# Kernel optimization log

Measured on AMD Instinct MI355X. Metric: run time of the kernel, lower is better.

Reference implementation:

```python
import jax, jax.numpy as jnp
import numpy as np

EPS = 1e-5
K_NEIGH = 8


def _conv1(x, w, b):
    # x: [B,C,N], w: [O,C], b: [O] -> [B,O,N]  (1x1 Conv1d)
    return jnp.einsum('bcn,oc->bon', x, w) + b[None, :, None]


def _bn(x, g, b):
    # BatchNorm1d in training mode: stats over (B, N)
    m = jnp.mean(x, axis=(0, 2), keepdims=True)
    v = jnp.var(x, axis=(0, 2), keepdims=True)
    return g[None, :, None] * (x - m) * jax.lax.rsqrt(v + EPS) + b[None, :, None]


def _get_local_diffs(x, k):
    # x: [B,N,C] -> [B, 2C, N]
    xyz = x[:, :, :3]
    sq = jnp.sum(xyz * xyz, axis=-1)  # [B,N]
    d2 = sq[:, :, None] + sq[:, None, :] - 2.0 * jnp.einsum('bnc,bmc->bnm', xyz, xyz)
    dists = jnp.sqrt(jnp.maximum(d2, 0.0))  # [B,N,N]
    _, idx = jax.lax.top_k(-dists, k + 1)   # smallest distances
    idx = idx[:, :, 1:]                     # drop self -> [B,N,k]
    neigh = jax.vmap(lambda xi, ii: xi[ii])(x, idx)  # [B,N,k,C]
    diff_mean = jnp.mean(neigh, axis=2) - x          # [B,N,C]
    out = jnp.concatenate([diff_mean, x], axis=2)    # [B,N,2C]
    return jnp.transpose(out, (0, 2, 1))             # [B,2C,N]


def _forward(x, w1, b1, g1, be1, w2, b2, g2, be2, w3, b3, g3, be3,
             qw, qb, kw, kb, vw, vb, fw, fb, aw1, ab1, aw2, ab2, fcw, fcb):
    h = _get_local_diffs(x, K_NEIGH)                 # [B,18,N]
    h = jax.nn.relu(_bn(_conv1(h, w1, b1), g1, be1))  # [B,64,N]
    h = jax.nn.relu(_bn(_conv1(h, w2, b2), g2, be2))  # [B,128,N]
    h = jax.nn.relu(_bn(_conv1(h, w3, b3), g3, be3))  # [B,256,N]
    # global attention
    Q = _conv1(h, qw, qb)  # [B,H,N]
    Kt = _conv1(h, kw, kb)
    V = _conv1(h, vw, vb)
    attn = jax.nn.softmax(jnp.einsum('bhn,bhm->bnm', Q, Kt), axis=-1)  # [B,N,N]
    o = jnp.einsum('bhm,bnm->bhn', V, attn)
    h = _conv1(o, fw, fb) + h
    # attention pooling
    a = jax.nn.relu(_conv1(h, aw1, ab1))
    s = _conv1(a, aw2, ab2)                 # [B,1,N]
    w = jax.nn.softmax(s, axis=-1)
    pooled = jnp.sum(h * w, axis=-1)        # [B,256]
    return jax.nn.relu(pooled @ fcw.T + fcb)  # [B,256]


def setup_inputs() -> dict:
    key = jax.random.key(0)
    ks = jax.random.split(key, 32)
    B, N, C = 4, 4096, 9
    HID = 128

    def p(i, shape, scale=0.05):
        return (jax.random.normal(ks[i], shape, dtype=jnp.float32) * scale)

    inp = {'x': jax.random.normal(ks[0], (B, N, C), dtype=jnp.float32)}
    dims = [(2 * C, 64), (64, 128), (128, 256)]
    for li, (ci, co) in enumerate(dims, start=1):
        inp[f'w{li}'] = p(li, (co, ci))
        inp[f'b{li}'] = p(li + 3, (co,))
        inp[f'g{li}'] = jnp.ones((co,), jnp.float32)
        inp[f'be{li}'] = jnp.zeros((co,), jnp.float32)
    Cf = 256
    inp['qw'] = p(7, (HID, Cf)); inp['qb'] = p(8, (HID,))
    inp['kw'] = p(9, (HID, Cf)); inp['kb'] = p(10, (HID,))
    inp['vw'] = p(11, (HID, Cf)); inp['vb'] = p(12, (HID,))
    inp['fw'] = p(13, (Cf, HID)); inp['fb'] = p(14, (Cf,))
    inp['aw1'] = p(15, (64, Cf)); inp['ab1'] = p(16, (64,))
    inp['aw2'] = p(17, (1, 64)); inp['ab2'] = p(18, (1,))
    inp['fcw'] = p(19, (256, Cf)); inp['fcb'] = p(20, (256,))
    return inp


def reference(x, w1, b1, g1, be1, w2, b2, g2, be2, w3, b3, g3, be3,
              qw, qb, kw, kb, vw, vb, fw, fb, aw1, ab1, aw2, ab2, fcw, fcb):
    return _forward(x, w1, b1, g1, be1, w2, b2, g2, be2, w3, b3, g3, be3,
                    qw, qb, kw, kb, vw, vb, fw, fb, aw1, ab1, aw2, ab2, fcw, fcb)
```

## Files before the change

kernel.cpp:

```cpp
#include <hip/hip_runtime.h>
#include <math.h>

constexpr int B    = 4;
constexpr int NPTS = 4096;
constexpr int NTOT = B * NPTS;
constexpr int CIN  = 9;
constexpr int C0   = 18;
constexpr int KNB  = 8;
constexpr int HID  = 128;
constexpr int QR   = 64;
constexpr int KC   = 64;
constexpr int NSPL = 4;
constexpr float EPSF = 1e-5f;

using f32x4  = __attribute__((ext_vector_type(4))) float;
using bf16x8 = __attribute__((ext_vector_type(8))) short;

__device__ inline unsigned short f2bf(float f) {
    unsigned int x = __float_as_uint(f);
    unsigned int r = (x + 0x7fffu + ((x >> 16) & 1u)) >> 16;
    return (unsigned short)r;
}
__device__ inline float bf2f(unsigned short u) {
    return __uint_as_float(((unsigned int)u) << 16);
}
__device__ inline unsigned int pack2(float a, float b) {
    return (unsigned int)f2bf(a) | ((unsigned int)f2bf(b) << 16);
}

#define GLD_LDS16(g, l) __builtin_amdgcn_global_load_lds( \
    (const __attribute__((address_space(1))) void*)(g),   \
    (__attribute__((address_space(3))) void*)(l), 16, 0, 0)

__global__ __launch_bounds__(256) void prep_kernel(const float* __restrict__ x,
                                                   float4* __restrict__ xyzw,
                                                   const float* __restrict__ w2,
                                                   const float* __restrict__ w3,
                                                   const float* __restrict__ qw,
                                                   const float* __restrict__ kw,
                                                   const float* __restrict__ vw,
                                                   const float* __restrict__ fw,
                                                   const float* __restrict__ aw1,
                                                   unsigned short* __restrict__ dst) {
    const int i = blockIdx.x * 256 + threadIdx.x;
    if (i < NTOT) {
        const float* xp = x + (size_t)i * CIN;
        const float a = xp[0], b = xp[1], c = xp[2];
        xyzw[i] = make_float4(a, b, c, a * a + b * b + c * c);
    }
    const float* src;
    int off;
    if      (i <   8192) { src = w2;  off = 0; }
    else if (i <  40960) { src = w3;  off = 8192; }
    else if (i <  73728) { src = qw;  off = 40960; }
    else if (i < 106496) { src = kw;  off = 73728; }
    else if (i < 139264) { src = vw;  off = 106496; }
    else if (i < 172032) { src = fw;  off = 139264; }
    else                 { src = aw1; off = 172032; }
    dst[i] = f2bf(src[i - off]);
}

__global__ __launch_bounds__(256) void knn3_kernel(const float* __restrict__ x,
                                                   const float4* __restrict__ xyzw,
                                                   float* __restrict__ h0) {
    __shared__ __align__(16) char lds[16384];
    const int tid = threadIdx.x;
    const int w = tid >> 6, l = tid & 63;
    const int b  = blockIdx.x >> 9;
    const int p0 = (blockIdx.x & 511) << 3;
    const int c  = l & 31;
    const int p  = w * 2 + (l >> 5);
    const int n  = p0 + p;
    const float4* xb4 = xyzw + (size_t)b * NPTS;

    const float4 q4 = xb4[n];
    const float qx = q4.x, qy = q4.y, qz = q4.z, sqn = q4.w;

    float bd[KNB];
    int   bi[KNB];
#pragma unroll
    for (int i = 0; i < KNB; ++i) { bd[i] = 3.0e38f; bi[i] = 0; }

    auto stage = [&](int buf, int t) {
#pragma unroll
        for (int i = 0; i < 2; ++i) {
            const int idx = i * 256 + w * 64 + l;
            const int m   = idx ^ ((idx >> 4) & 7);
            GLD_LDS16(xb4 + (size_t)t * 512 + m, lds + buf * 8192 + i * 4096 + w * 1024);
        }
    };

    stage(0, 0);
    for (int t = 0; t < 8; ++t) {
        const int cur = t & 1;
        __syncthreads();
        if (t < 7) stage(cur ^ 1, t + 1);

        float thr = bd[KNB - 1];
        thr = fminf(thr, __shfl_xor(thr, 1));
        thr = fminf(thr, __shfl_xor(thr, 2));
        thr = fminf(thr, __shfl_xor(thr, 4));
        thr = fminf(thr, __shfl_xor(thr, 8));
        thr = fminf(thr, __shfl_xor(thr, 16));

        float gate = fminf(thr, bd[KNB - 1]);
        const char* buf = lds + cur * 8192 + c * 256;
        const int mbase = t * 512 + c * 16;
        const int cswz  = (c & 7) << 4;
#pragma unroll 4
        for (int j = 0; j < 16; ++j) {
            const float4 f4 = *(const float4*)(buf + ((j << 4) ^ cswz));
            const float tt = fmaf(qx, f4.x, fmaf(qy, f4.y, qz * f4.z));
            const float d2 = fmaf(-2.0f, tt, sqn + f4.w);
            const int m = mbase + j;
            const bool want = (d2 < gate) && (m != n);
            if (__any(want)) {
                if (want) {
                    bd[KNB - 1] = d2; bi[KNB - 1] = m;
#pragma unroll
                    for (int s = KNB - 1; s > 0; --s) {
                        if (bd[s] < bd[s - 1]) {
                            float td = bd[s]; bd[s] = bd[s - 1]; bd[s - 1] = td;
                            int   ti = bi[s]; bi[s] = bi[s - 1]; bi[s - 1] = ti;
                        }
                    }
                }
                gate = fminf(thr, bd[KNB - 1]);
            }
        }
    }

    int res[KNB];
    const int lh = l & 31;
#pragma unroll
    for (int r = 0; r < KNB; ++r) {
        float hd = bd[0]; int hb = bi[0]; int hl = lh;
#pragma unroll
        for (int mask = 16; mask > 0; mask >>= 1) {
            const float od = __shfl_xor(hd, mask);
            const int   ob = __shfl_xor(hb, mask);
            const int   ol = __shfl_xor(hl, mask);
            if (od < hd || (od == hd && ol < hl)) { hd = od; hb = ob; hl = ol; }
        }
        res[r] = hb;
        if (lh == hl) {
#pragma unroll
            for (int s = 0; s < KNB - 1; ++s) { bd[s] = bd[s + 1]; bi[s] = bi[s + 1]; }
            bd[KNB - 1] = 3.0e38f;
        }
    }

    const int c8 = c & 7;
    int nb = res[0];
#pragma unroll
    for (int k = 1; k < KNB; ++k) nb = (c8 == k) ? res[k] : nb;
    const float* xb = x + (size_t)b * NPTS * CIN;
    float nv[CIN];
    const float* nbp = xb + (size_t)nb * CIN;
#pragma unroll
    for (int ch = 0; ch < CIN; ++ch) nv[ch] = nbp[ch];
#pragma unroll
    for (int d = 1; d < 8; d <<= 1) {
#pragma unroll
        for (int ch = 0; ch < CIN; ++ch) nv[ch] += __shfl_xor(nv[ch], d);
    }
    const int ch = min(c, 8);
    float nvc = nv[0];
#pragma unroll
    for (int k = 1; k < CIN; ++k) nvc = (ch == k) ? nv[k] : nvc;
    if (c < 9) {
        const float xv = xb[(size_t)n * CIN + ch];
        h0[((size_t)b * C0 + ch) * NPTS + n]       = nvc * 0.125f - xv;
        h0[((size_t)b * C0 + CIN + ch) * NPTS + n] = xv;
    }
}

__global__ __launch_bounds__(256) void conv1_kernel(const float* __restrict__ X,
                                                    const float* __restrict__ W,
                                                    const float* __restrict__ bias,
                                                    float* __restrict__ Y,
                                                    float* __restrict__ parts) {
    __shared__ float Ws[16 * C0];
    const int b  = blockIdx.z;
    const int o_base = blockIdx.y * 16;
    const int l  = threadIdx.x & 63;
    const int n  = blockIdx.x * 64 + l;
    const int og = threadIdx.x >> 6;
    for (int i = threadIdx.x; i < 16 * C0; i += 256)
        Ws[i] = W[(size_t)o_base * C0 + i];
    __syncthreads();
    float acc[4] = {0.f, 0.f, 0.f, 0.f};
    const float* Xp = X + (size_t)b * C0 * NPTS + n;
    for (int c = 0; c < C0; ++c) {
        const float xv = Xp[(size_t)c * NPTS];
#pragma unroll
        for (int i = 0; i < 4; ++i)
            acc[i] = fmaf(Ws[(og * 4 + i) * C0 + c], xv, acc[i]);
    }
    f32x4 v;
#pragma unroll
    for (int i = 0; i < 4; ++i) v[i] = acc[i] + bias[o_base + og * 4 + i];
    *(f32x4*)(Y + ((size_t)b * NPTS + n) * 64 + o_base + og * 4) = v;
    float s1[4], s2[4];
#pragma unroll
    for (int i = 0; i < 4; ++i) { s1[i] = v[i]; s2[i] = v[i] * v[i]; }
#pragma unroll
    for (int d = 1; d < 64; d <<= 1) {
#pragma unroll
        for (int i = 0; i < 4; ++i) {
            s1[i] += __shfl_xor(s1[i], d);
            s2[i] += __shfl_xor(s2[i], d);
        }
    }
    if (l == 0) {
        const int rg = blockIdx.z * 64 + blockIdx.x;
#pragma unroll
        for (int i = 0; i < 4; ++i) {
            const int ch = o_base + og * 4 + i;
            parts[ch * 256 + rg]            = s1[i];
            parts[64 * 256 + ch * 256 + rg] = s2[i];
        }
    }
}

__global__ __launch_bounds__(64) void finstats_kernel(const float* __restrict__ parts,
                                                      float* __restrict__ mstats, int O) {
    const int ch = blockIdx.x, l = threadIdx.x;
    const f32x4 a1 = *(const f32x4*)(parts + (size_t)ch * 256 + l * 4);
    const f32x4 a2 = *(const f32x4*)(parts + (size_t)O * 256 + (size_t)ch * 256 + l * 4);
    float s1 = (a1[0] + a1[1]) + (a1[2] + a1[3]);
    float s2 = (a2[0] + a2[1]) + (a2[2] + a2[3]);
#pragma unroll
    for (int d = 1; d < 64; d <<= 1) {
        s1 += __shfl_xor(s1, d);
        s2 += __shfl_xor(s2, d);
    }
    if (l == 0) {
        const float mean = s1 * (1.0f / NTOT);
        const float var  = s2 * (1.0f / NTOT) - mean * mean;
        mstats[ch]     = mean;
        mstats[O + ch] = rsqrtf(var + EPSF);
    }
}

__global__ __launch_bounds__(256) void bnapply_kernel(const float* __restrict__ Y,
                                                      const float* __restrict__ mstats,
                                                      const float* __restrict__ g,
                                                      const float* __restrict__ be,
                                                      unsigned short* __restrict__ Yb,
                                                      int O) {
    const size_t i4 = (size_t)blockIdx.x * 256 + threadIdx.x;
    const int cbase = (int)((i4 * 4) & (O - 1));
    const f32x4 v = *(const f32x4*)(Y + i4 * 4);
    ushort4 pk;
    unsigned short* pp = (unsigned short*)&pk;
#pragma unroll
    for (int r = 0; r < 4; ++r) {
        const int c = cbase + r;
        const float y = fmaxf(g[c] * mstats[O + c] * (v[r] - mstats[c]) + be[c], 0.f);
        pp[r] = f2bf(y);
    }
    *(ushort4*)(Yb + i4 * 4) = pk;
}

template <int C, int EPI>
__global__ __launch_bounds__(256) void gemm_kernel(const unsigned short* __restrict__ A,
                                                   const unsigned short* __restrict__ Wb,
                                                   const float* __restrict__ bias,
                                                   const unsigned short* __restrict__ resid,
                                                   void* __restrict__ Yv, int O,
                                                   float* __restrict__ parts) {
    constexpr int RB = 2 * C;
    constexpr int SLOTS = C / 8;
    __shared__ __align__(16) char ldsW[64 * RB];
    const int tid = threadIdx.x;
    const int w = tid >> 6, l = tid & 63;
    const int lg = l >> 4, lq = l & 15;
    const int n0 = blockIdx.x * 64;
    const int o0 = blockIdx.y * 64;

#pragma unroll
    for (int i = 0; i < C / 32; ++i) {
        const int idx = i * 256 + tid;
        const int m  = idx / SLOTS;
        const int sl = (idx % SLOTS) ^ (m & 7);
        GLD_LDS16(Wb + (size_t)(o0 + m) * C + sl * 8, ldsW + (i * 256 + w * 64) * 16);
    }

    const int nr = n0 + w * 16 + lq;
    const unsigned short* Ap = A + (size_t)nr * C + lg * 8;
    f32x4 acc[4];
#pragma unroll
    for (int os = 0; os < 4; ++os) acc[os] = {0.f, 0.f, 0.f, 0.f};
    __syncthreads();

#pragma unroll
    for (int ks = 0; ks < C / 32; ++ks) {
        const bf16x8 af = *(const bf16x8*)(Ap + ks * 32);
#pragma unroll
        for (int os = 0; os < 4; ++os) {
            const int row = os * 16 + lq;
            const bf16x8 wf = *(const bf16x8*)(ldsW + ((row * RB + ks * 64 + lg * 16) ^ ((lq & 7) << 4)));
            acc[os] = __builtin_amdgcn_mfma_f32_16x16x32_bf16(wf, af, acc[os], 0, 0, 0);
        }
    }

    f32x4 vv[4];
    float dotacc = 0.f;
#pragma unroll
    for (int os = 0; os < 4; ++os) {
        const int ob = o0 + os * 16 + lg * 4;
        const f32x4 bv = *(const f32x4*)(bias + ob);
#pragma unroll
        for (int r = 0; r < 4; ++r) vv[os][r] = acc[os][r] + bv[r];
        if (EPI == 0) {
            *(f32x4*)((float*)Yv + (size_t)nr * O + ob) = vv[os];
        } else if (EPI == 4) {
            unsigned short* Y = (unsigned short*)Yv;
            const int bb = nr >> 12, n = nr & (NPTS - 1);
#pragma unroll
            for (int r = 0; r < 4; ++r)
                Y[((size_t)bb * HID + ob + r) * NPTS + n] = f2bf(vv[os][r]);
        } else if (EPI == 5) {
            const f32x4 w2v = *(const f32x4*)((const float*)resid + ob);
#pragma unroll
            for (int r = 0; r < 4; ++r)
                dotacc = fmaf(fmaxf(vv[os][r], 0.f), w2v[r], dotacc);
        } else {
            f32x4 v = vv[os];
            if (EPI == 3) {
                const ushort4 rv = *(const ushort4*)(resid + (size_t)nr * O + ob);
                v[0] += bf2f(rv.x); v[1] += bf2f(rv.y); v[2] += bf2f(rv.z); v[3] += bf2f(rv.w);
            }
            if (EPI == 2) {
#pragma unroll
                for (int r = 0; r < 4; ++r) v[r] = fmaxf(v[r], 0.f);
            }
            ushort4 pk;
            pk.x = f2bf(v[0]); pk.y = f2bf(v[1]); pk.z = f2bf(v[2]); pk.w = f2bf(v[3]);
            *(ushort4*)((unsigned short*)Yv + (size_t)nr * O + ob) = pk;
        }
    }

    if (EPI == 5) {
        dotacc += __shfl_xor(dotacc, 16);
        dotacc += __shfl_xor(dotacc, 32);
        if (lg == 0) ((float*)Yv)[nr] = dotacc + ((const float*)parts)[0];
    }

    if (EPI == 0) {
        float* sred = (float*)ldsW;
        float s1[4][4], s2[4][4];
#pragma unroll
        for (int os = 0; os < 4; ++os)
#pragma unroll
            for (int r = 0; r < 4; ++r) {
                float a1 = vv[os][r], a2 = vv[os][r] * vv[os][r];
#pragma unroll
                for (int d = 1; d < 16; d <<= 1) {
                    a1 += __shfl_xor(a1, d);
                    a2 += __shfl_xor(a2, d);
                }
                s1[os][r] = a1; s2[os][r] = a2;
            }
        __syncthreads();
        if (lq == 0) {
#pragma unroll
            for (int os = 0; os < 4; ++os)
#pragma unroll
                for (int r = 0; r < 4; ++r) {
                    const int ch = os * 16 + lg * 4 + r;
                    sred[(w * 64 + ch) * 2 + 0] = s1[os][r];
                    sred[(w * 64 + ch) * 2 + 1] = s2[os][r];
                }
        }
        __syncthreads();
        if (tid < 128) {
            const int ch = tid & 63, st = tid >> 6;
            const float a = sred[ch * 2 + st] + sred[(64 + ch) * 2 + st]
                          + sred[(128 + ch) * 2 + st] + sred[(192 + ch) * 2 + st];
            parts[(size_t)st * O * 256 + (size_t)(o0 + ch) * 256 + blockIdx.x] = a;
        }
    }
}

__global__ __launch_bounds__(256) void qkv_kernel(const unsigned short* __restrict__ A,
                                                  const unsigned short* __restrict__ Wall,
                                                  const float* __restrict__ qb,
                                                  const float* __restrict__ kb,
                                                  const float* __restrict__ vb,
                                                  unsigned short* __restrict__ Qo,
                                                  unsigned short* __restrict__ Ko,
                                                  unsigned short* __restrict__ Vo) {
    constexpr int C = 256, RB = 512, SLOTS = 32;
    __shared__ __align__(16) char ldsW[64 * RB];
    const int tid = threadIdx.x;
    const int w = tid >> 6, l = tid & 63;
    const int lg = l >> 4, lq = l & 15;
    const int n0 = blockIdx.x * 64;
    const int by = blockIdx.y;
    const int proj = by >> 1;
    const int o0 = (by & 1) * 64;
    const unsigned short* Wb = Wall + (size_t)proj * 32768;
    const float* bias = (proj == 0) ? qb : (proj == 1) ? kb : vb;

#pragma unroll
    for (int i = 0; i < C / 32; ++i) {
        const int idx = i * 256 + tid;
        const int m  = idx / SLOTS;
        const int sl = (idx % SLOTS) ^ (m & 7);
        GLD_LDS16(Wb + (size_t)(o0 + m) * C + sl * 8, ldsW + (i * 256 + w * 64) * 16);
    }

    const int nr = n0 + w * 16 + lq;
    const unsigned short* Ap = A + (size_t)nr * C + lg * 8;
    f32x4 acc[4];
#pragma unroll
    for (int os = 0; os < 4; ++os) acc[os] = {0.f, 0.f, 0.f, 0.f};
    __syncthreads();

#pragma unroll
    for (int ks = 0; ks < C / 32; ++ks) {
        const bf16x8 af = *(const bf16x8*)(Ap + ks * 32);
#pragma unroll
        for (int os = 0; os < 4; ++os) {
            const int row = os * 16 + lq;
            const bf16x8 wf = *(const bf16x8*)(ldsW + ((row * RB + ks * 64 + lg * 16) ^ ((lq & 7) << 4)));
            acc[os] = __builtin_amdgcn_mfma_f32_16x16x32_bf16(wf, af, acc[os], 0, 0, 0);
        }
    }

#pragma unroll
    for (int os = 0; os < 4; ++os) {
        const int ob = o0 + os * 16 + lg * 4;
        const f32x4 bv = *(const f32x4*)(bias + ob);
        f32x4 v;
#pragma unroll
        for (int r = 0; r < 4; ++r) v[r] = acc[os][r] + bv[r];
        if (proj < 2) {
            unsigned short* Y = proj ? Ko : Qo;
            ushort4 pk;
            pk.x = f2bf(v[0]); pk.y = f2bf(v[1]); pk.z = f2bf(v[2]); pk.w = f2bf(v[3]);
            *(ushort4*)(Y + (size_t)nr * 128 + ob) = pk;
        } else {
            const int bb = nr >> 12, n = nr & (NPTS - 1);
#pragma unroll
            for (int r = 0; r < 4; ++r)
                Vo[((size_t)bb * HID + ob + r) * NPTS + n] = f2bf(v[r]);
        }
    }
}

__device__ __forceinline__ void stage_tile(char* lds, int buf,
                                           const unsigned short* Kb,
                                           const unsigned short* Vb,
                                           int n0, int w, int l) {
    char* dK = lds + buf * 16384;
    char* dV = lds + 32768 + buf * 16384;
#pragma unroll
    for (int j = 0; j < 4; ++j) {
        const int y = w * 4096 + j * 1024 + l * 16;
        const int m = y >> 8;
        const int slot = ((y >> 4) & 15) ^ (m & 7);
        GLD_LDS16(Kb + (size_t)(n0 + m) * HID + slot * 8, dK + w * 4096 + j * 1024);
    }
#pragma unroll
    for (int j = 0; j < 4; ++j) {
        const int y = w * 4096 + j * 1024 + l * 16;
        const int h = y >> 7;
        const int slot = ((y >> 4) & 7) ^ (h & 7);
        GLD_LDS16(Vb + (size_t)h * NPTS + n0 + slot * 8, dV + w * 4096 + j * 1024);
    }
}

__global__ __launch_bounds__(256) void fmha2_kernel(const unsigned short* __restrict__ Qg,
                                                    const unsigned short* __restrict__ Kg,
                                                    const unsigned short* __restrict__ Vg,
                                                    float* __restrict__ A0, float* __restrict__ A1,
                                                    float* __restrict__ A2, float* __restrict__ A3,
                                                    float* __restrict__ Mb, float* __restrict__ Lb) {
    __shared__ __align__(16) char lds[73728];
    const int tid = threadIdx.x;
    const int w = tid >> 6, l = tid & 63;
    const int lg = l >> 4, lq = l & 15;
    const int b  = blockIdx.y;
    const int q0 = blockIdx.x * QR;
    const int split = blockIdx.z;
    const int n0base = split * (NPTS / NSPL);
    float* Ap = (split == 0) ? A0 : (split == 1) ? A1 : (split == 2) ? A2 : A3;
    float* Mp = Mb + split * NTOT;
    float* Lp = Lb + split * NTOT;
    char* ldsP = lds + 65536 + w * 2048;

    bf16x8 qf[4];
    {
        const unsigned short* qp = Qg + ((size_t)b * NPTS + q0 + w * 16 + lq) * HID + lg * 8;
#pragma unroll
        for (int ks = 0; ks < 4; ++ks)
            qf[ks] = *(const bf16x8*)(qp + ks * 32);
    }
    const unsigned short* Kb = Kg + (size_t)b * NPTS * HID;
    const unsigned short* Vb = Vg + (size_t)b * HID * NPTS;

    float m_r = -3.0e38f;
    float lsum = 0.f;
    f32x4 oacc[8];
#pragma unroll
    for (int hs = 0; hs < 8; ++hs) oacc[hs] = {0.f, 0.f, 0.f, 0.f};

    constexpr int NT = (NPTS / NSPL) / KC;
    stage_tile(lds, 0, Kb, Vb, n0base, w, l);

    for (int t = 0; t < NT; ++t) {
        const int cur = t & 1;
        __syncthreads();
        if (t + 1 < NT)
            stage_tile(lds, cur ^ 1, Kb, Vb, n0base + (t + 1) * KC, w, l);
        char* ldsK = lds + cur * 16384;
        char* ldsV = lds + 32768 + cur * 16384;

        f32x4 sv[4];
        __builtin_amdgcn_s_setprio(1);
#pragma unroll
        for (int ms = 0; ms < 4; ++ms) {
            const int row = ms * 16 + lq;
            f32x4 s = {0.f, 0.f, 0.f, 0.f};
#pragma unroll
            for (int ks = 0; ks < 4; ++ks) {
                bf16x8 kf = *(const bf16x8*)(ldsK + ((row * 256 + ks * 64 + lg * 16) ^ ((row & 7) << 4)));
                s = __builtin_amdgcn_mfma_f32_16x16x32_bf16(kf, qf[ks], s, 0, 0, 0);
            }
            sv[ms] = s;
        }
        __builtin_amdgcn_s_setprio(0);

        float pmax = sv[0][0];
#pragma unroll
        for (int ms = 0; ms < 4; ++ms)
#pragma unroll
            for (int r = 0; r < 4; ++r) pmax = fmaxf(pmax, sv[ms][r]);
        pmax = fmaxf(pmax, __shfl_xor(pmax, 16));
        pmax = fmaxf(pmax, __shfl_xor(pmax, 32));

        if (__any(pmax > m_r + 8.0f)) {
            const float newm = fmaxf(m_r, pmax);
            const float sc = __expf(m_r - newm);
            lsum *= sc;
            float sc_r[4];
#pragma unroll
            for (int r = 0; r < 4; ++r) sc_r[r] = __shfl(sc, lg * 4 + r);
#pragma unroll
            for (int hs = 0; hs < 8; ++hs)
#pragma unroll
                for (int r = 0; r < 4; ++r) oacc[hs][r] *= sc_r[r];
            m_r = newm;
        }

#pragma unroll
        for (int ms = 0; ms < 4; ++ms) {
            const float p0 = __expf(sv[ms][0] - m_r);
            const float p1 = __expf(sv[ms][1] - m_r);
            const float p2 = __expf(sv[ms][2] - m_r);
            const float p3 = __expf(sv[ms][3] - m_r);
            lsum += (p0 + p1) + (p2 + p3);
            const int lin = lq * 128 + ms * 32 + lg * 8;
            const int ad  = lin ^ ((lq & 7) << 4);
            *(unsigned int*)(ldsP + ad)     = pack2(p0, p1);
            *(unsigned int*)(ldsP + ad + 4) = pack2(p2, p3);
        }

        __builtin_amdgcn_s_setprio(1);
#pragma unroll
        for (int msl = 0; msl < 2; ++msl) {
            bf16x8 pf = *(const bf16x8*)(ldsP + ((lq * 128 + msl * 64 + lg * 16) ^ ((lq & 7) << 4)));
#pragma unroll
            for (int hs = 0; hs < 8; ++hs) {
                const int hrow = hs * 16 + lq;
                bf16x8 vf = *(const bf16x8*)(ldsV + ((hrow * 128 + msl * 64 + lg * 16) ^ ((hrow & 7) << 4)));
                oacc[hs] = __builtin_amdgcn_mfma_f32_16x16x32_bf16(pf, vf, oacc[hs], 0, 0, 0);
            }
        }
        __builtin_amdgcn_s_setprio(0);
    }

    lsum += __shfl_xor(lsum, 16);
    lsum += __shfl_xor(lsum, 32);
    float* Ab = Ap + ((size_t)b * NPTS + q0 + w * 16) * HID;
#pragma unroll
    for (int hs = 0; hs < 8; ++hs) {
#pragma unroll
        for (int r = 0; r < 4; ++r)
            Ab[(size_t)(lg * 4 + r) * HID + hs * 16 + lq] = oacc[hs][r];
    }
    if (lg == 0) {
        Mp[b * NPTS + q0 + w * 16 + lq] = m_r;
        Lp[b * NPTS + q0 + w * 16 + lq] = lsum;
    }
}

__global__ __launch_bounds__(256) void fmha_combine_kernel(const float* __restrict__ A0,
                                                           const float* __restrict__ A1,
                                                           const float* __restrict__ A2,
                                                           const float* __restrict__ A3,
                                                           const float* __restrict__ Mb,
                                                           const float* __restrict__ Lb,
                                                           unsigned short* __restrict__ Ob) {
    const int i = blockIdx.x * 256 + threadIdx.x;
    const int nidx = i >> 7;
    const float m0 = Mb[nidx], m1 = Mb[NTOT + nidx];
    const float m2 = Mb[2 * NTOT + nidx], m3 = Mb[3 * NTOT + nidx];
    const float M = fmaxf(fmaxf(m0, m1), fmaxf(m2, m3));
    const float e0 = __expf(m0 - M), e1 = __expf(m1 - M);
    const float e2 = __expf(m2 - M), e3 = __expf(m3 - M);
    const float den = e0 * Lb[nidx] + e1 * Lb[NTOT + nidx]
                    + e2 * Lb[2 * NTOT + nidx] + e3 * Lb[3 * NTOT + nidx];
    const float num = e0 * A0[i] + e1 * A1[i] + e2 * A2[i] + e3 * A3[i];
    Ob[i] = f2bf(num / den);
}

__global__ __launch_bounds__(256) void softmax_w_kernel(float* __restrict__ s) {
    const int b = blockIdx.x;
    const int tid = threadIdx.x;
    __shared__ float red[256];
    float lm = -3.0e38f;
    for (int n = tid; n < NPTS; n += 256) lm = fmaxf(lm, s[b * NPTS + n]);
    red[tid] = lm;
    __syncthreads();
    for (int st = 128; st > 0; st >>= 1) {
        if (tid < st) red[tid] = fmaxf(red[tid], red[tid + st]);
        __syncthreads();
    }
    const float mx = red[0];
    __syncthreads();
    float ls = 0.f;
    for (int n = tid; n < NPTS; n += 256) {
        const float p = __expf(s[b * NPTS + n] - mx);
        s[b * NPTS + n] = p;
        ls += p;
    }
    red[tid] = ls;
    __syncthreads();
    for (int st = 128; st > 0; st >>= 1) {
        if (tid < st) red[tid] += red[tid + st];
        __syncthreads();
    }
    const float inv = 1.f / red[0];
    __syncthreads();
    for (int n = tid; n < NPTS; n += 256) s[b * NPTS + n] *= inv;
}

__global__ __launch_bounds__(256) void pool3_kernel(const unsigned short* __restrict__ h,
                                                    const float* __restrict__ w,
                                                    float* __restrict__ pooled) {
    const int b  = blockIdx.y;
    const int n0 = blockIdx.x * 64;
    const int cg = (threadIdx.x & 63) * 4;
    const int rs = threadIdx.x >> 6;
    float a0 = 0.f, a1 = 0.f, a2 = 0.f, a3 = 0.f;
#pragma unroll 4
    for (int i = 0; i < 16; ++i) {
        const int n = n0 + i * 4 + rs;
        const ushort4 v = *(const ushort4*)(h + ((size_t)b * NPTS + n) * 256 + cg);
        const float wv = w[b * NPTS + n];
        a0 = fmaf(bf2f(v.x), wv, a0);
        a1 = fmaf(bf2f(v.y), wv, a1);
        a2 = fmaf(bf2f(v.z), wv, a2);
        a3 = fmaf(bf2f(v.w), wv, a3);
    }
    float* pp = pooled + b * 256 + cg;
    atomicAdd(pp + 0, a0);
    atomicAdd(pp + 1, a1);
    atomicAdd(pp + 2, a2);
    atomicAdd(pp + 3, a3);
}

__global__ __launch_bounds__(256) void fc_kernel(const float* __restrict__ pooled,
                                                 const float* __restrict__ fcw,
                                                 const float* __restrict__ fcb,
                                                 float* __restrict__ out) {
    const int b = blockIdx.x, j = threadIdx.x;
    __shared__ float ps[256];
    ps[j] = pooled[b * 256 + j];
    __syncthreads();
    float acc = fcb[j];
    for (int c = 0; c < 256; ++c) acc = fmaf(ps[c], fcw[j * 256 + c], acc);
    out[b * 256 + j] = fmaxf(acc, 0.f);
}

extern "C" void kernel_launch(void* const* d_in, const int* in_sizes, int n_in,
                              void* d_out, int out_size, void* d_ws, size_t ws_size,
                              hipStream_t stream) {
    const float* x   = (const float*)d_in[0];
    const float* w1  = (const float*)d_in[1];
    const float* b1  = (const float*)d_in[2];
    const float* g1  = (const float*)d_in[3];
    const float* be1 = (const float*)d_in[4];
    const float* w2  = (const float*)d_in[5];
    const float* b2  = (const float*)d_in[6];
    const float* g2  = (const float*)d_in[7];
    const float* be2 = (const float*)d_in[8];
    const float* w3  = (const float*)d_in[9];
    const float* b3  = (const float*)d_in[10];
    const float* g3  = (const float*)d_in[11];
    const float* be3 = (const float*)d_in[12];
    const float* qw  = (const float*)d_in[13];
    const float* qb  = (const float*)d_in[14];
    const float* kw  = (const float*)d_in[15];
    const float* kb  = (const float*)d_in[16];
    const float* vw  = (const float*)d_in[17];
    const float* vb  = (const float*)d_in[18];
    const float* fw  = (const float*)d_in[19];
    const float* fb  = (const float*)d_in[20];
    const float* aw1 = (const float*)d_in[21];
    const float* ab1 = (const float*)d_in[22];
    const float* aw2 = (const float*)d_in[23];
    const float* ab2 = (const float*)d_in[24];
    const float* fcw = (const float*)d_in[25];
    const float* fcb = (const float*)d_in[26];

    float* ws = (float*)d_ws;
    float* h0     = ws;
    float* arena1 = h0 + 294912;
    float* arena2 = arena1 + 4194304;
    float* arena3 = arena2 + 2097152;
    float* arena4 = arena3 + 1048576;
    float* arena5 = arena4 + 1048576;
    float* arena6 = arena5 + 1048576;
    float* arena7 = arena6 + 2097152;
    float* Mls    = arena7 + 2097152;
    float* s      = Mls + 131072;
    float* pooled = s + 16384;
    float* mstats = pooled + 1024;
    float* wbf    = mstats + 512;
    float* xyzwp  = wbf + 94208;
    float* parts  = xyzwp + 65536;

    float* y1 = arena1;
    float* y2 = arena1;
    float* y3 = arena1;
    unsigned short* H1b = (unsigned short*)arena3;
    unsigned short* H2b = (unsigned short*)arena3;
    unsigned short* Qb  = (unsigned short*)arena3;
    unsigned short* OBF = (unsigned short*)arena3;
    unsigned short* H3b = (unsigned short*)arena2;
    unsigned short* Kb  = (unsigned short*)arena4;
    unsigned short* Vb  = (unsigned short*)arena5;
    float* Acc0 = arena6;
    unsigned short* H4b = (unsigned short*)arena6;
    float* Acc1 = arena7;
    float* Acc2 = arena1;
    float* Acc3 = arena1 + 2097152;
    float* Mb = Mls;
    float* Lb = Mls + 4 * NTOT;
    unsigned short* WB = (unsigned short*)wbf;
    unsigned short* w2b  = WB;
    unsigned short* w3b  = WB + 8192;
    unsigned short* qwb  = WB + 40960;
    unsigned short* fwb  = WB + 139264;
    unsigned short* aw1b = WB + 172032;
    float4* xyzw = (float4*)xyzwp;

    hipMemsetAsync(pooled, 0, 1024 * sizeof(float), stream);
    prep_kernel<<<dim3(736), 256, 0, stream>>>(x, xyzw, w2, w3, qw, kw, vw, fw, aw1, WB);
    knn3_kernel<<<dim3(NTOT / 8), 256, 0, stream>>>(x, xyzw, h0);

    conv1_kernel<<<dim3(NPTS / 64, 4, B), 256, 0, stream>>>(h0, w1, b1, y1, parts);
    finstats_kernel<<<64, 64, 0, stream>>>(parts, mstats, 64);
    bnapply_kernel<<<dim3(NTOT * 64 / 1024), 256, 0, stream>>>(y1, mstats, g1, be1, H1b, 64);
    gemm_kernel<64, 0><<<dim3(NTOT / 64, 2), 256, 0, stream>>>(H1b, w2b, b2, nullptr, y2, 128, parts);
    finstats_kernel<<<128, 64, 0, stream>>>(parts, mstats, 128);
    bnapply_kernel<<<dim3(NTOT * 128 / 1024), 256, 0, stream>>>(y2, mstats, g2, be2, H2b, 128);
    gemm_kernel<128, 0><<<dim3(NTOT / 64, 4), 256, 0, stream>>>(H2b, w3b, b3, nullptr, y3, 256, parts);
    finstats_kernel<<<256, 64, 0, stream>>>(parts, mstats, 256);
    bnapply_kernel<<<dim3(NTOT * 256 / 1024), 256, 0, stream>>>(y3, mstats, g3, be3, H3b, 256);

    qkv_kernel<<<dim3(NTOT / 64, 6), 256, 0, stream>>>(H3b, qwb, qb, kb, vb, Qb, Kb, Vb);

    fmha2_kernel<<<dim3(NPTS / QR, B, NSPL), 256, 0, stream>>>(Qb, Kb, Vb, Acc0, Acc1, Acc2, Acc3, Mb, Lb);
    fmha_combine_kernel<<<dim3(NTOT * HID / 256), 256, 0, stream>>>(Acc0, Acc1, Acc2, Acc3, Mb, Lb, OBF);

    gemm_kernel<128, 3><<<dim3(NTOT / 64, 4), 256, 0, stream>>>(OBF, fwb, fb, H3b, H4b, 256, nullptr);
    gemm_kernel<256, 5><<<dim3(NTOT / 64, 1), 256, 0, stream>>>(H4b, aw1b, ab1,
                                                                (const unsigned short*)aw2, s, 64, (float*)ab2);

    softmax_w_kernel<<<B, 256, 0, stream>>>(s);
    pool3_kernel<<<dim3(64, B), 256, 0, stream>>>(H4b, s, pooled);
    fc_kernel<<<B, 256, 0, stream>>>(pooled, fcw, fcb, (float*)d_out);

    (void)in_sizes; (void)n_in; (void)out_size; (void)ws_size;
}
```

Measured before the change: 287.6 us.

## Pack distance and index into sortable keys with branchless top-k insertion

The kNN selection now packs each candidate's distance (mantissa truncated to 20 bits) and its 12-bit point index into one unsigned key. Every candidate is inserted through a branchless min/max chain, replacing the gated, wave-voted branchy insertion. The cross-lane merge also becomes a single integer min-reduction. This removes divergence, per-tile threshold shuffles and duplicated index registers. In exchange it does a full compare-swap chain for every candidate, and truncating the distance can reorder near-equal neighbours.

```diff
diff --git a/kernel.cpp b/kernel.cpp
--- a/kernel.cpp
+++ b/kernel.cpp
@@ -69,17 +69,15 @@
     const int b  = blockIdx.x >> 9;
     const int p0 = (blockIdx.x & 511) << 3;
     const int c  = l & 31;
-    const int p  = w * 2 + (l >> 5);
-    const int n  = p0 + p;
+    const int n  = p0 + w * 2 + (l >> 5);
     const float4* xb4 = xyzw + (size_t)b * NPTS;
 
     const float4 q4 = xb4[n];
     const float qx = q4.x, qy = q4.y, qz = q4.z, sqn = q4.w;
 
-    float bd[KNB];
-    int   bi[KNB];
-#pragma unroll
-    for (int i = 0; i < KNB; ++i) { bd[i] = 3.0e38f; bi[i] = 0; }
+    unsigned int bd[KNB];
+#pragma unroll
+    for (int i = 0; i < KNB; ++i) bd[i] = 0xFFFFFFFFu;
 
     auto stage = [&](int buf, int t) {
 #pragma unroll
@@ -96,14 +94,6 @@
         __syncthreads();
         if (t < 7) stage(cur ^ 1, t + 1);
 
-        float thr = bd[KNB - 1];
-        thr = fminf(thr, __shfl_xor(thr, 1));
-        thr = fminf(thr, __shfl_xor(thr, 2));
-        thr = fminf(thr, __shfl_xor(thr, 4));
-        thr = fminf(thr, __shfl_xor(thr, 8));
-        thr = fminf(thr, __shfl_xor(thr, 16));
-
-        float gate = fminf(thr, bd[KNB - 1]);
         const char* buf = lds + cur * 8192 + c * 256;
         const int mbase = t * 512 + c * 16;
         const int cswz  = (c & 7) << 4;
@@ -111,49 +101,40 @@
         for (int j = 0; j < 16; ++j) {
             const float4 f4 = *(const float4*)(buf + ((j << 4) ^ cswz));
             const float tt = fmaf(qx, f4.x, fmaf(qy, f4.y, qz * f4.z));
-            const float d2 = fmaf(-2.0f, tt, sqn + f4.w);
+            const float d2 = fmaxf(fmaf(-2.0f, tt, sqn + f4.w), 0.f);
             const int m = mbase + j;
-            const bool want = (d2 < gate) && (m != n);
-            if (__any(want)) {
-                if (want) {
-                    bd[KNB - 1] = d2; bi[KNB - 1] = m;
-#pragma unroll
-                    for (int s = KNB - 1; s > 0; --s) {
-                        if (bd[s] < bd[s - 1]) {
-                            float td = bd[s]; bd[s] = bd[s - 1]; bd[s - 1] = td;
-                            int   ti = bi[s]; bi[s] = bi[s - 1]; bi[s - 1] = ti;
-                        }
-                    }
-                }
-                gate = fminf(thr, bd[KNB - 1]);
+            unsigned int key = (__float_as_uint(d2) & 0xFFFFF000u) | (unsigned int)m;
+            if (m == n) key = 0xFFFFFFFFu;
+            bd[KNB - 1] = min(bd[KNB - 1], key);
+#pragma unroll
+            for (int s = KNB - 1; s > 0; --s) {
+                const unsigned int lo = min(bd[s - 1], bd[s]);
+                const unsigned int hi = max(bd[s - 1], bd[s]);
+                bd[s - 1] = lo; bd[s] = hi;
             }
         }
     }
 
-    int res[KNB];
-    const int lh = l & 31;
+    unsigned int res[KNB];
 #pragma unroll
     for (int r = 0; r < KNB; ++r) {
-        float hd = bd[0]; int hb = bi[0]; int hl = lh;
-#pragma unroll
-        for (int mask = 16; mask > 0; mask >>= 1) {
-            const float od = __shfl_xor(hd, mask);
-            const int   ob = __shfl_xor(hb, mask);
-            const int   ol = __shfl_xor(hl, mask);
-            if (od < hd || (od == hd && ol < hl)) { hd = od; hb = ob; hl = ol; }
-        }
-        res[r] = hb;
-        if (lh == hl) {
-#pragma unroll
-            for (int s = 0; s < KNB - 1; ++s) { bd[s] = bd[s + 1]; bi[s] = bi[s + 1]; }
-            bd[KNB - 1] = 3.0e38f;
+        unsigned int v = bd[0];
+#pragma unroll
+        for (int mask = 16; mask > 0; mask >>= 1)
+            v = min(v, (unsigned int)__shfl_xor((int)v, mask));
+        res[r] = v;
+        if (bd[0] == v) {
+#pragma unroll
+            for (int s = 0; s < KNB - 1; ++s) bd[s] = bd[s + 1];
+            bd[KNB - 1] = 0xFFFFFFFFu;
         }
     }
 
     const int c8 = c & 7;
-    int nb = res[0];
-#pragma unroll
-    for (int k = 1; k < KNB; ++k) nb = (c8 == k) ? res[k] : nb;
+    unsigned int kk = res[0];
+#pragma unroll
+    for (int k = 1; k < KNB; ++k) kk = (c8 == k) ? res[k] : kk;
+    const int nb = (int)(kk & 0xFFFu);
     const float* xb = x + (size_t)b * NPTS * CIN;
     float nv[CIN];
     const float* nbp = xb + (size_t)nb * CIN;
```

Measured after the change: 248.3 us. 13.7% less time.
